# Kernel optimization log

Measured on AMD Instinct MI355X. Metric: run time of the kernel, lower is better.

## Reference

```python
import jax, jax.numpy as jnp
import numpy as np

N, E, H, C, IN = 50000, 500000, 4, 64, 256


def setup_inputs() -> dict:
    key = jax.random.key(0)
    ks = jax.random.split(key, 16)
    sW = 1.0 / np.sqrt(IN)
    sA = 1.0 / np.sqrt(C)
    inp = {
        "x": jax.random.normal(ks[0], (N, IN), jnp.float32),
        "edge_index": jax.random.randint(ks[1], (2, E), 0, N, jnp.int64 if jax.config.jax_enable_x64 else jnp.int32),
        "W1": jax.random.normal(ks[2], (IN, H * C), jnp.float32) * sW,
        "as1": jax.random.normal(ks[3], (H, C), jnp.float32) * sA,
        "ad1": jax.random.normal(ks[4], (H, C), jnp.float32) * sA,
        "b1": jnp.zeros((H * C,), jnp.float32),
        "W2": jax.random.normal(ks[5], (H * C, H * C), jnp.float32) * sW,
        "as2": jax.random.normal(ks[6], (H, C), jnp.float32) * sA,
        "ad2": jax.random.normal(ks[7], (H, C), jnp.float32) * sA,
        "b2": jnp.zeros((H * C,), jnp.float32),
        "WN": jax.random.normal(ks[8], (H * C, H * C), jnp.float32) * sW,
        "asN": jax.random.normal(ks[9], (H, C), jnp.float32) * sA,
        "adN": jax.random.normal(ks[10], (H, C), jnp.float32) * sA,
        "bN": jnp.zeros((H * C,), jnp.float32),
    }
    return inp


def _gat_conv(x, src, dst, W, a_src, a_dst, b, n_nodes):
    # x: [N, F_in]; src/dst: [E'] (self-loops included); W: [F_in, H*C]
    Hh, Cc = a_src.shape
    h = (x @ W).reshape(n_nodes, Hh, Cc)                      # [N,H,C]
    e_src = jnp.einsum("nhc,hc->nh", h, a_src)                # [N,H]
    e_dst = jnp.einsum("nhc,hc->nh", h, a_dst)
    e = jax.nn.leaky_relu(e_src[src] + e_dst[dst], 0.2)       # [E',H]
    m = jax.lax.stop_gradient(jax.ops.segment_max(e, dst, num_segments=n_nodes))
    ex = jnp.exp(e - m[dst])
    denom = jax.ops.segment_sum(ex, dst, num_segments=n_nodes)
    alpha = ex / (denom[dst] + 1e-16)                         # [E',H]
    out = jax.ops.segment_sum(h[src] * alpha[:, :, None], dst, num_segments=n_nodes)
    return out.reshape(n_nodes, Hh * Cc) + b


def reference(x, edge_index, W1, as1, ad1, b1, W2, as2, ad2, b2, WN, asN, adN, bN):
    n = x.shape[0]
    loops = jnp.arange(n, dtype=edge_index.dtype)
    src = jnp.concatenate([edge_index[0], loops])  # PyG GATConv add_self_loops=True
    dst = jnp.concatenate([edge_index[1], loops])
    inp = x
    h = jax.nn.relu(_gat_conv(x, src, dst, W1, as1, ad1, b1, n)) + inp
    h = jax.nn.relu(_gat_conv(h, src, dst, W2, as2, ad2, b2, n))
    h = _gat_conv(h, src, dst, WN, asN, adN, bN, n)
    # eval mode: F.dropout is identity
    return jax.nn.relu(h + inp)
```

## Files before the change

kernel.cpp:

```cpp
#include <hip/hip_runtime.h>
#include <hip/hip_bf16.h>
#include <math.h>

typedef short short8 __attribute__((ext_vector_type(8)));
typedef float f32x4 __attribute__((ext_vector_type(4)));

static __device__ __forceinline__ float bfu(unsigned short u) {
    union { unsigned int i; float f; } c; c.i = ((unsigned int)u) << 16; return c.f;
}
static __device__ __forceinline__ ushort f2bu(float f) {
    __hip_bfloat16 h = __float2bfloat16(f);
    return *(ushort*)&h;
}


__global__ void k_wt_cast3(const float* __restrict__ W1, const float* __restrict__ W2,
                           const float* __restrict__ W3, __hip_bfloat16* __restrict__ Wt1,
                           __hip_bfloat16* __restrict__ Wt2, __hip_bfloat16* __restrict__ Wt3) {
    int n = blockIdx.x, k = threadIdx.x;
    const float* W = (blockIdx.y == 0) ? W1 : (blockIdx.y == 1) ? W2 : W3;
    __hip_bfloat16* Wt = (blockIdx.y == 0) ? Wt1 : (blockIdx.y == 1) ? Wt2 : Wt3;
    Wt[n * 256 + k] = __float2bfloat16(W[k * 256 + n]);
}


__global__ void k_set1(int* a, int n) {
    int i = blockIdx.x * blockDim.x + threadIdx.x;
    if (i < n) a[i] = 1;
}

__global__ void k_hist(const int* __restrict__ dstv, int* __restrict__ cnt, int E) {
    int i = blockIdx.x * blockDim.x + threadIdx.x;
    if (i < E) atomicAdd(&cnt[dstv[i]], 1);
}

__global__ void k_scan1(const int* __restrict__ cnt, int* __restrict__ excl, int* __restrict__ bsum, int n) {
    __shared__ int s[256];
    int i = blockIdx.x * 256 + threadIdx.x;
    int v = (i < n) ? cnt[i] : 0;
    s[threadIdx.x] = v;
    __syncthreads();
    for (int off = 1; off < 256; off <<= 1) {
        int t = (threadIdx.x >= off) ? s[threadIdx.x - off] : 0;
        __syncthreads();
        s[threadIdx.x] += t;
        __syncthreads();
    }
    if (i < n) excl[i] = s[threadIdx.x] - v;
    if (threadIdx.x == 255) bsum[blockIdx.x] = s[255];
}

__global__ void k_scan2(const int* __restrict__ bsum, int* __restrict__ boff, int nb) {
    __shared__ int s[256];
    int carry = 0;
    for (int base = 0; base < nb; base += 256) {
        int i = base + threadIdx.x;
        int v = (i < nb) ? bsum[i] : 0;
        s[threadIdx.x] = v;
        __syncthreads();
        for (int off = 1; off < 256; off <<= 1) {
            int t = (threadIdx.x >= off) ? s[threadIdx.x - off] : 0;
            __syncthreads();
            s[threadIdx.x] += t;
            __syncthreads();
        }
        if (i < nb) boff[i] = carry + s[threadIdx.x] - v;
        carry += s[255];
        __syncthreads();
    }
}

__global__ void k_scan3(const int* __restrict__ excl, const int* __restrict__ boff,
                        int* __restrict__ rowptr, int* __restrict__ cursor, int n, int Etot) {
    int i = blockIdx.x * blockDim.x + threadIdx.x;
    if (i < n) {
        int v = excl[i] + boff[i >> 8];
        rowptr[i] = v;
        cursor[i] = v;
    }
    if (i == 0) rowptr[n] = Etot;
}

__global__ void k_scatter(const int* __restrict__ srcv, const int* __restrict__ dstv,
                          int* __restrict__ cursor, int* __restrict__ colsrc, int E, int Nn) {
    int i = blockIdx.x * blockDim.x + threadIdx.x;
    if (i < E) {
        int pos = atomicAdd(&cursor[dstv[i]], 1);
        colsrc[pos] = srcv[i];
    } else if (i < E + Nn) {
        int nn = i - E;
        int pos = atomicAdd(&cursor[nn], 1);
        colsrc[pos] = nn;
    }
}


template <bool AFP32>
__global__ __launch_bounds__(256) void k_gemm(const void* __restrict__ Ap,
                                              const __hip_bfloat16* __restrict__ Wt,
                                              __hip_bfloat16* __restrict__ C,
                                              const float* __restrict__ a_src,
                                              const float* __restrict__ a_dst,
                                              float* __restrict__ es,
                                              float* __restrict__ ed, int M) {
    __shared__ __align__(16) char As[64 * 128];
    __shared__ __align__(16) char Bs[256 * 128];
    int tid = threadIdx.x;
    int w = tid >> 6, l = tid & 63;
    int m0 = blockIdx.x * 64;
    f32x4 acc[4][4];
#pragma unroll
    for (int a = 0; a < 4; ++a)
#pragma unroll
        for (int b = 0; b < 4; ++b) acc[a][b] = (f32x4){0.f, 0.f, 0.f, 0.f};

    for (int bk = 0; bk < 256; bk += 64) {
        __syncthreads();
#pragma unroll
        for (int i = 0; i < 2; ++i) {
            int c = tid + 256 * i;
            int row = c >> 3, ko = c & 7;
            int rg = m0 + row;
            uint4 v = {0u, 0u, 0u, 0u};
            if (rg < M) {
                if (AFP32) {
                    const float* Af = (const float*)Ap;
                    float4 f0 = *(const float4*)(Af + (size_t)rg * 256 + bk + ko * 8);
                    float4 f1 = *(const float4*)(Af + (size_t)rg * 256 + bk + ko * 8 + 4);
                    v.x = (uint)f2bu(f0.x) | ((uint)f2bu(f0.y) << 16);
                    v.y = (uint)f2bu(f0.z) | ((uint)f2bu(f0.w) << 16);
                    v.z = (uint)f2bu(f1.x) | ((uint)f2bu(f1.y) << 16);
                    v.w = (uint)f2bu(f1.z) | ((uint)f2bu(f1.w) << 16);
                } else {
                    v = *(const uint4*)((const char*)Ap + (size_t)rg * 512 + bk * 2 + ko * 16);
                }
            }
            int off = (ko * 16) ^ ((row & 7) << 4);
            *(uint4*)(As + row * 128 + off) = v;
        }
#pragma unroll
        for (int i = 0; i < 8; ++i) {
            int c = tid + 256 * i;
            int row = c >> 3, ko = c & 7;
            uint4 v = *(const uint4*)((const char*)Wt + (size_t)row * 512 + bk * 2 + ko * 16);
            int off = (ko * 16) ^ ((row & 7) << 4);
            *(uint4*)(Bs + row * 128 + off) = v;
        }
        __syncthreads();
        int lo = l & 15, hi = l >> 4;
#pragma unroll
        for (int kk = 0; kk < 2; ++kk) {
            int koff = kk * 64 + hi * 16;
            short8 af[4], bfr[4];
#pragma unroll
            for (int mi = 0; mi < 4; ++mi) {
                int row = mi * 16 + lo;
                af[mi] = *(const short8*)(As + row * 128 + (koff ^ ((row & 7) << 4)));
            }
#pragma unroll
            for (int ni = 0; ni < 4; ++ni) {
                int row = w * 64 + ni * 16 + lo;
                bfr[ni] = *(const short8*)(Bs + row * 128 + (koff ^ ((row & 7) << 4)));
            }
#pragma unroll
            for (int mi = 0; mi < 4; ++mi)
#pragma unroll
                for (int ni = 0; ni < 4; ++ni)
                    acc[mi][ni] = __builtin_amdgcn_mfma_f32_16x16x32_bf16(af[mi], bfr[ni], acc[mi][ni], 0, 0, 0);
        }
    }
    int lo = l & 15, hi = l >> 4;
#pragma unroll
    for (int mi = 0; mi < 4; ++mi) {
#pragma unroll
        for (int r = 0; r < 4; ++r) {
            int rg = m0 + mi * 16 + hi * 4 + r;
            if (rg < M) {
#pragma unroll
                for (int ni = 0; ni < 4; ++ni) {
                    int col = w * 64 + ni * 16 + lo;
                    C[(size_t)rg * 256 + col] = __float2bfloat16(acc[mi][ni][r]);
                }
            }
        }
    }
    float avv[4], adv[4];
#pragma unroll
    for (int ni = 0; ni < 4; ++ni) {
        avv[ni] = a_src[w * 64 + ni * 16 + lo];
        adv[ni] = a_dst[w * 64 + ni * 16 + lo];
    }
#pragma unroll
    for (int mi = 0; mi < 4; ++mi) {
#pragma unroll
        for (int r = 0; r < 4; ++r) {
            int rg = m0 + mi * 16 + hi * 4 + r;
            float s1 = 0.f, s2 = 0.f;
#pragma unroll
            for (int ni = 0; ni < 4; ++ni) {
                s1 += acc[mi][ni][r] * avv[ni];
                s2 += acc[mi][ni][r] * adv[ni];
            }
#pragma unroll
            for (int mk = 1; mk < 16; mk <<= 1) {
                s1 += __shfl_xor(s1, mk, 64);
                s2 += __shfl_xor(s2, mk, 64);
            }
            if (lo == 0 && rg < M) {
                es[rg * 4 + w] = s1;
                ed[rg * 4 + w] = s2;
            }
        }
    }
}


__global__ __launch_bounds__(256) void k_aggregate(const __hip_bfloat16* __restrict__ hW,
                            const int* __restrict__ rowptr,
                            const int* __restrict__ colsrc, const float* __restrict__ es,
                            const float* __restrict__ edv_, const float* __restrict__ bias,
                            const float* __restrict__ xres, __hip_bfloat16* __restrict__ outbf,
                            float* __restrict__ outf, int mode, int Nn) {
    int n = blockIdx.x * 4 + (threadIdx.x >> 6);
    if (n >= Nn) return;
    int l = threadIdx.x & 63;
    int h = l >> 4;
    int r0 = rowptr[n];
    int deg = rowptr[n + 1] - r0;
    float edv = edv_[n * 4 + h];

    float denom = 0.f;
    float a0 = 0.f, a1 = 0.f, a2 = 0.f, a3 = 0.f;
    const ushort* hw = (const ushort*)hW;
    int sfb = colsrc[r0];

    for (int base = 0; base < deg; base += 8) {
        int sv[8];
#pragma unroll
        for (int u = 0; u < 8; ++u)
            sv[u] = (base + u < deg) ? colsrc[r0 + base + u] : sfb;
        float ev[8];
#pragma unroll
        for (int u = 0; u < 8; ++u)
            ev[u] = es[(size_t)sv[u] * 4 + h];
        uint2 hv[8];
#pragma unroll
        for (int u = 0; u < 8; ++u)
            hv[u] = *(const uint2*)(hw + (size_t)sv[u] * 256 + l * 4);
#pragma unroll
        for (int u = 0; u < 8; ++u) {
            float t = ev[u] + edv;
            t = fmaxf(t, 0.2f * t);
            float p = (base + u < deg) ? __expf(t) : 0.f;
            denom += p;
            a0 += p * bfu((ushort)(hv[u].x & 0xffff));
            a1 += p * bfu((ushort)(hv[u].x >> 16));
            a2 += p * bfu((ushort)(hv[u].y & 0xffff));
            a3 += p * bfu((ushort)(hv[u].y >> 16));
        }
    }

    float inv = 1.f / (denom + 1e-16f);
    int idx = n * 256 + l * 4;
    float4 b4 = *(const float4*)(bias + l * 4);
    float v0 = a0 * inv + b4.x;
    float v1 = a1 * inv + b4.y;
    float v2 = a2 * inv + b4.z;
    float v3 = a3 * inv + b4.w;

    if (mode == 2) {
        float4 x4 = *(const float4*)(xres + idx);
        float4 o;
        o.x = fmaxf(v0 + x4.x, 0.f);
        o.y = fmaxf(v1 + x4.y, 0.f);
        o.z = fmaxf(v2 + x4.z, 0.f);
        o.w = fmaxf(v3 + x4.w, 0.f);
        *(float4*)(outf + idx) = o;
    } else {
        v0 = fmaxf(v0, 0.f); v1 = fmaxf(v1, 0.f);
        v2 = fmaxf(v2, 0.f); v3 = fmaxf(v3, 0.f);
        if (mode == 0) {
            float4 x4 = *(const float4*)(xres + idx);
            v0 += x4.x; v1 += x4.y; v2 += x4.z; v3 += x4.w;
        }
        union { ushort u[4]; uint2 v; } o;
        o.u[0] = f2bu(v0); o.u[1] = f2bu(v1);
        o.u[2] = f2bu(v2); o.u[3] = f2bu(v3);
        *(uint2*)((ushort*)outbf + idx) = o.v;
    }
}


extern "C" void kernel_launch(void* const* d_in, const int* in_sizes, int n_in,
                              void* d_out, int out_size, void* d_ws, size_t ws_size,
                              hipStream_t stream) {
    const float* x  = (const float*)d_in[0];
    const int* ei   = (const int*)d_in[1];
    const float* W1 = (const float*)d_in[2];
    const float* as1 = (const float*)d_in[3];
    const float* ad1 = (const float*)d_in[4];
    const float* b1  = (const float*)d_in[5];
    const float* W2  = (const float*)d_in[6];
    const float* as2 = (const float*)d_in[7];
    const float* ad2 = (const float*)d_in[8];
    const float* b2  = (const float*)d_in[9];
    const float* WN  = (const float*)d_in[10];
    const float* asN = (const float*)d_in[11];
    const float* adN = (const float*)d_in[12];
    const float* bN  = (const float*)d_in[13];

    int Nn = in_sizes[0] / 256;
    int E = in_sizes[1] / 2;
    const int* srcv = ei;
    const int* dstv = ei + E;
    int Etot = E + Nn;

    char* p = (char*)d_ws;
    auto alloc = [&](size_t bytes) {
        char* r = p;
        p += (bytes + 255) & ~(size_t)255;
        return r;
    };
    __hip_bfloat16* Pbf  = (__hip_bfloat16*)alloc((size_t)Nn * 256 * 2);
    __hip_bfloat16* Qbf  = (__hip_bfloat16*)alloc((size_t)Nn * 256 * 2);
    __hip_bfloat16* hWbf = (__hip_bfloat16*)alloc((size_t)Nn * 256 * 2);
    __hip_bfloat16* Wt1  = (__hip_bfloat16*)alloc(256 * 256 * 2);
    __hip_bfloat16* Wt2  = (__hip_bfloat16*)alloc(256 * 256 * 2);
    __hip_bfloat16* Wt3  = (__hip_bfloat16*)alloc(256 * 256 * 2);
    float* esrc = (float*)alloc((size_t)Nn * 4 * 4);
    float* edst = (float*)alloc((size_t)Nn * 4 * 4);
    int* cnt    = (int*)alloc((size_t)Nn * 4);
    int* excl   = (int*)alloc((size_t)Nn * 4);
    int* rowptr = (int*)alloc((size_t)(Nn + 1) * 4);
    int* cursor = (int*)alloc((size_t)Nn * 4);
    int* bsum   = (int*)alloc(4096);
    int* boff   = (int*)alloc(4096);
    int* colsrc = (int*)alloc((size_t)Etot * 4);

    int nb = (Nn + 255) / 256;

    dim3 wg(256, 3);
    k_wt_cast3<<<wg, 256, 0, stream>>>(W1, W2, WN, Wt1, Wt2, Wt3);

    k_set1<<<nb, 256, 0, stream>>>(cnt, Nn);
    k_hist<<<(E + 255) / 256, 256, 0, stream>>>(dstv, cnt, E);
    k_scan1<<<nb, 256, 0, stream>>>(cnt, excl, bsum, Nn);
    k_scan2<<<1, 256, 0, stream>>>(bsum, boff, nb);
    k_scan3<<<nb, 256, 0, stream>>>(excl, boff, rowptr, cursor, Nn, Etot);
    k_scatter<<<(Etot + 255) / 256, 256, 0, stream>>>(srcv, dstv, cursor, colsrc, E, Nn);

    int gg = (Nn + 63) / 64;
    int ga = (Nn + 3) / 4;

    k_gemm<true><<<gg, 256, 0, stream>>>(x, Wt1, hWbf, as1, ad1, esrc, edst, Nn);
    k_aggregate<<<ga, 256, 0, stream>>>(hWbf, rowptr, colsrc, esrc, edst, b1, x, Pbf, nullptr, 0, Nn);
    k_gemm<false><<<gg, 256, 0, stream>>>(Pbf, Wt2, hWbf, as2, ad2, esrc, edst, Nn);
    k_aggregate<<<ga, 256, 0, stream>>>(hWbf, rowptr, colsrc, esrc, edst, b2, x, Qbf, nullptr, 1, Nn);
    k_gemm<false><<<gg, 256, 0, stream>>>(Qbf, Wt3, hWbf, asN, adN, esrc, edst, Nn);
    k_aggregate<<<ga, 256, 0, stream>>>(hWbf, rowptr, colsrc, esrc, edst, bN, x, nullptr, (float*)d_out, 2, Nn);
}
```

Baseline: 300.3 us.

## Keep weight fragments in registers and load full-K A tile once in GEMM

The GEMM now loads each wave's B (weight) fragments straight from global memory into registers for the whole K=256, and stages the full 64x256 A tile in shared memory once. This replaces the four-step K loop, which reloaded B through shared memory with two barriers per step. Occupancy is set to two blocks per SIMD via launch bounds, which costs heavy register pressure from the 32 short8 B fragments. The weight transpose-cast kernel also switches to a tiled shared-memory transpose so its global reads and writes are coalesced.

New measurement: 323.1 us. 7.6% more time.

```diff
diff --git a/kernel.cpp b/kernel.cpp
--- a/kernel.cpp
+++ b/kernel.cpp
@@ -14,13 +14,26 @@
 }
 
 
-__global__ void k_wt_cast3(const float* __restrict__ W1, const float* __restrict__ W2,
+__global__ __launch_bounds__(256) void k_wt_cast3(const float* __restrict__ W1, const float* __restrict__ W2,
                            const float* __restrict__ W3, __hip_bfloat16* __restrict__ Wt1,
                            __hip_bfloat16* __restrict__ Wt2, __hip_bfloat16* __restrict__ Wt3) {
-    int n = blockIdx.x, k = threadIdx.x;
-    const float* W = (blockIdx.y == 0) ? W1 : (blockIdx.y == 1) ? W2 : W3;
-    __hip_bfloat16* Wt = (blockIdx.y == 0) ? Wt1 : (blockIdx.y == 1) ? Wt2 : Wt3;
-    Wt[n * 256 + k] = __float2bfloat16(W[k * 256 + n]);
+    __shared__ float t[64][65];
+    const float* W = (blockIdx.z == 0) ? W1 : (blockIdx.z == 1) ? W2 : W3;
+    __hip_bfloat16* Wt = (blockIdx.z == 0) ? Wt1 : (blockIdx.z == 1) ? Wt2 : Wt3;
+    int k0 = blockIdx.x * 64, n0 = blockIdx.y * 64;
+#pragma unroll
+    for (int i = 0; i < 16; ++i) {
+        int idx = threadIdx.x + 256 * i;
+        int r = idx >> 6, c = idx & 63;
+        t[r][c] = W[(size_t)(k0 + r) * 256 + n0 + c];
+    }
+    __syncthreads();
+#pragma unroll
+    for (int i = 0; i < 16; ++i) {
+        int idx = threadIdx.x + 256 * i;
+        int r = idx >> 6, c = idx & 63;
+        Wt[(size_t)(n0 + r) * 256 + k0 + c] = __float2bfloat16(t[c][r]);
+    }
 }
 
 
@@ -96,80 +109,69 @@
 
 
 template <bool AFP32>
-__global__ __launch_bounds__(256) void k_gemm(const void* __restrict__ Ap,
+__global__ __launch_bounds__(256, 2) void k_gemm(const void* __restrict__ Ap,
                                               const __hip_bfloat16* __restrict__ Wt,
                                               __hip_bfloat16* __restrict__ C,
                                               const float* __restrict__ a_src,
                                               const float* __restrict__ a_dst,
                                               float* __restrict__ es,
                                               float* __restrict__ ed, int M) {
-    __shared__ __align__(16) char As[64 * 128];
-    __shared__ __align__(16) char Bs[256 * 128];
+    __shared__ __align__(16) char As[64 * 512];
     int tid = threadIdx.x;
     int w = tid >> 6, l = tid & 63;
+    int lo = l & 15, hi = l >> 4;
     int m0 = blockIdx.x * 64;
+
+    short8 bfr[4][8];
+#pragma unroll
+    for (int ni = 0; ni < 4; ++ni)
+#pragma unroll
+        for (int kk = 0; kk < 8; ++kk)
+            bfr[ni][kk] = *(const short8*)((const char*)Wt +
+                (size_t)(w * 64 + ni * 16 + lo) * 512 + kk * 64 + hi * 16);
+
+#pragma unroll
+    for (int i = 0; i < 8; ++i) {
+        int c = tid + 256 * i;
+        int row = c >> 5, ko = c & 31;
+        int rg = m0 + row;
+        uint4 v = {0u, 0u, 0u, 0u};
+        if (rg < M) {
+            if (AFP32) {
+                const float* Af = (const float*)Ap;
+                float4 f0 = *(const float4*)(Af + (size_t)rg * 256 + ko * 8);
+                float4 f1 = *(const float4*)(Af + (size_t)rg * 256 + ko * 8 + 4);
+                v.x = (uint)f2bu(f0.x) | ((uint)f2bu(f0.y) << 16);
+                v.y = (uint)f2bu(f0.z) | ((uint)f2bu(f0.w) << 16);
+                v.z = (uint)f2bu(f1.x) | ((uint)f2bu(f1.y) << 16);
+                v.w = (uint)f2bu(f1.z) | ((uint)f2bu(f1.w) << 16);
+            } else {
+                v = *(const uint4*)((const char*)Ap + (size_t)rg * 512 + ko * 16);
+            }
+        }
+        *(uint4*)(As + row * 512 + ((ko * 16) ^ ((row & 7) << 4))) = v;
+    }
+    __syncthreads();
+
     f32x4 acc[4][4];
 #pragma unroll
     for (int a = 0; a < 4; ++a)
 #pragma unroll
         for (int b = 0; b < 4; ++b) acc[a][b] = (f32x4){0.f, 0.f, 0.f, 0.f};
 
-    for (int bk = 0; bk < 256; bk += 64) {
-        __syncthreads();
-#pragma unroll
-        for (int i = 0; i < 2; ++i) {
-            int c = tid + 256 * i;
-            int row = c >> 3, ko = c & 7;
-            int rg = m0 + row;
-            uint4 v = {0u, 0u, 0u, 0u};
-            if (rg < M) {
-                if (AFP32) {
-                    const float* Af = (const float*)Ap;
-                    float4 f0 = *(const float4*)(Af + (size_t)rg * 256 + bk + ko * 8);
-                    float4 f1 = *(const float4*)(Af + (size_t)rg * 256 + bk + ko * 8 + 4);
-                    v.x = (uint)f2bu(f0.x) | ((uint)f2bu(f0.y) << 16);
-                    v.y = (uint)f2bu(f0.z) | ((uint)f2bu(f0.w) << 16);
-                    v.z = (uint)f2bu(f1.x) | ((uint)f2bu(f1.y) << 16);
-                    v.w = (uint)f2bu(f1.z) | ((uint)f2bu(f1.w) << 16);
-                } else {
-                    v = *(const uint4*)((const char*)Ap + (size_t)rg * 512 + bk * 2 + ko * 16);
-                }
-            }
-            int off = (ko * 16) ^ ((row & 7) << 4);
-            *(uint4*)(As + row * 128 + off) = v;
-        }
-#pragma unroll
-        for (int i = 0; i < 8; ++i) {
-            int c = tid + 256 * i;
-            int row = c >> 3, ko = c & 7;
-            uint4 v = *(const uint4*)((const char*)Wt + (size_t)row * 512 + bk * 2 + ko * 16);
-            int off = (ko * 16) ^ ((row & 7) << 4);
-            *(uint4*)(Bs + row * 128 + off) = v;
-        }
-        __syncthreads();
-        int lo = l & 15, hi = l >> 4;
-#pragma unroll
-        for (int kk = 0; kk < 2; ++kk) {
-            int koff = kk * 64 + hi * 16;
-            short8 af[4], bfr[4];
-#pragma unroll
-            for (int mi = 0; mi < 4; ++mi) {
-                int row = mi * 16 + lo;
-                af[mi] = *(const short8*)(As + row * 128 + (koff ^ ((row & 7) << 4)));
-            }
-#pragma unroll
-            for (int ni = 0; ni < 4; ++ni) {
-                int row = w * 64 + ni * 16 + lo;
-                bfr[ni] = *(const short8*)(Bs + row * 128 + (koff ^ ((row & 7) << 4)));
-            }
-#pragma unroll
-            for (int mi = 0; mi < 4; ++mi)
-#pragma unroll
-                for (int ni = 0; ni < 4; ++ni)
-                    acc[mi][ni] = __builtin_amdgcn_mfma_f32_16x16x32_bf16(af[mi], bfr[ni], acc[mi][ni], 0, 0, 0);
-        }
-    }
-    int lo = l & 15, hi = l >> 4;
+#pragma unroll
+    for (int kk = 0; kk < 8; ++kk) {
+#pragma unroll
+        for (int mi = 0; mi < 4; ++mi) {
+            int row = mi * 16 + lo;
+            short8 af = *(const short8*)(As + row * 512 +
+                        ((kk * 64 + hi * 16) ^ ((row & 7) << 4)));
+#pragma unroll
+            for (int ni = 0; ni < 4; ++ni)
+                acc[mi][ni] = __builtin_amdgcn_mfma_f32_16x16x32_bf16(af, bfr[ni][kk], acc[mi][ni], 0, 0, 0);
+        }
+    }
+
 #pragma unroll
     for (int mi = 0; mi < 4; ++mi) {
 #pragma unroll
@@ -339,7 +341,7 @@
 
     int nb = (Nn + 255) / 256;
 
-    dim3 wg(256, 3);
+    dim3 wg(4, 4, 3);
     k_wt_cast3<<<wg, 256, 0, stream>>>(W1, W2, WN, Wt1, Wt2, Wt3);
 
     k_set1<<<nb, 256, 0, stream>>>(cnt, Nn);
```
